# Performance work log

Hardware: AMD Instinct MI355X
Metric: run time of the kernel (lower is better)

The kernel has to match this reference:

```python
import jax, jax.numpy as jnp
import numpy as np

D_MODEL = 256
N_LAYER = 4
D_INNER = 512   # expand=2
D_STATE = 16
DT_RANK = 16    # ceil(d_model/16)
D_CONV = 4
VOCAB = 16
BATCH = 1
SEQLEN = 4096
EPS = 1e-5


def setup_inputs() -> dict:
    key = jax.random.key(0)
    ks = jax.random.split(key, 10)
    s = 0.02
    A_init = jnp.log(jnp.arange(1, D_STATE + 1, dtype=jnp.float32))  # S4D-real init
    return {
        "input_ids": jax.random.randint(ks[0], (BATCH, SEQLEN), 0, VOCAB, dtype=jnp.int32),
        "embed_w": jax.random.normal(ks[1], (VOCAB, D_MODEL), jnp.float32) * s,
        "norm_w": jnp.ones((N_LAYER, D_MODEL), jnp.float32),
        "in_proj_w": jax.random.normal(ks[2], (N_LAYER, 2 * D_INNER, D_MODEL), jnp.float32) * s,
        "out_proj_w": jax.random.normal(ks[3], (N_LAYER, D_MODEL, D_INNER), jnp.float32) * s,
        "conv_w": jax.random.normal(ks[4], (N_LAYER, 2, D_INNER, D_CONV), jnp.float32) * s,
        "conv_b": jnp.zeros((N_LAYER, 2, D_INNER), jnp.float32),
        "x_proj_w": jax.random.normal(ks[5], (N_LAYER, 2, DT_RANK + 2 * D_STATE, D_INNER), jnp.float32) * s,
        "dt_proj_w": jax.random.normal(ks[6], (N_LAYER, 2, D_INNER, DT_RANK), jnp.float32) * s,
        "dt_proj_b": jax.random.normal(ks[7], (N_LAYER, 2, D_INNER), jnp.float32) * 0.1,
        "A_log": jnp.broadcast_to(A_init, (N_LAYER, 2, D_INNER, D_STATE)) + 0.0,
        "Dp": jnp.ones((N_LAYER, 2, D_INNER), jnp.float32),
        "norm_f_w": jnp.ones((D_MODEL,), jnp.float32),
    }


def rmsnorm(x, w):
    return x * jax.lax.rsqrt(jnp.mean(x * x, axis=-1, keepdims=True) + EPS) * w


def selective_scan(u, dt, A, Bm, Cm, Dv):
    # u, dt: (B,L,Di); A: (Di,N); Bm, Cm: (B,L,N); Dv: (Di,)
    dA = jnp.exp(dt[..., None] * A)                         # (B,L,Di,N)
    dBu = dt[..., None] * Bm[:, :, None, :] * u[..., None]  # (B,L,Di,N)

    def step(h, xs):
        dA_t, dBu_t, C_t = xs
        h = dA_t * h + dBu_t                                # (B,Di,N)
        y = jnp.einsum('bdn,bn->bd', h, C_t)
        return h, y

    h0 = jnp.zeros((u.shape[0], D_INNER, D_STATE), u.dtype)
    xs = (jnp.moveaxis(dA, 1, 0), jnp.moveaxis(dBu, 1, 0), jnp.moveaxis(Cm, 1, 0))
    _, ys = jax.lax.scan(step, h0, xs)                      # (L,B,Di)
    return jnp.moveaxis(ys, 0, 1) + u * Dv


def mamba_dir(x, in_w, out_w, cw, cb, xpw, dtw, dtb, a_log, dv):
    # x: (B,L,D)
    xz = jnp.einsum('bld,ed->ble', x, in_w)                 # (B,L,2*Di)
    u, z = jnp.split(xz, 2, axis=-1)
    # causal depthwise conv1d
    uc = jnp.moveaxis(u, 1, 2)                              # (B,Di,L)
    uc = jax.lax.conv_general_dilated(
        uc, cw[:, None, :], (1,), [(D_CONV - 1, 0)],
        feature_group_count=D_INNER, dimension_numbers=('NCH', 'OIH', 'NCH'))
    u = jax.nn.silu(jnp.moveaxis(uc, 1, 2) + cb)            # (B,L,Di)
    xdb = jnp.einsum('bld,ed->ble', u, xpw)                 # (B,L,dt_rank+2N)
    dt_r, Bm, Cm = jnp.split(xdb, [DT_RANK, DT_RANK + D_STATE], axis=-1)
    dt = jax.nn.softplus(jnp.einsum('blr,dr->bld', dt_r, dtw) + dtb)
    A = -jnp.exp(a_log)                                     # (Di,N)
    y = selective_scan(u, dt, A, Bm, Cm, dv)
    y = y * jax.nn.silu(z)
    return jnp.einsum('bld,od->blo', y, out_w)


def reference(input_ids, embed_w, norm_w, in_proj_w, out_proj_w, conv_w, conv_b,
              x_proj_w, dt_proj_w, dt_proj_b, A_log, Dp, norm_f_w):
    h = embed_w[input_ids]                                  # (B,L,D)
    residual = None
    for i in range(N_LAYER):
        residual = h if residual is None else h + residual  # residual_in_fp32
        hn = rmsnorm(residual, norm_w[i])
        out_f = mamba_dir(hn, in_proj_w[i], out_proj_w[i], conv_w[i, 0], conv_b[i, 0],
                          x_proj_w[i, 0], dt_proj_w[i, 0], dt_proj_b[i, 0], A_log[i, 0], Dp[i, 0])
        out_r = mamba_dir(hn[:, ::-1], in_proj_w[i], out_proj_w[i], conv_w[i, 1], conv_b[i, 1],
                          x_proj_w[i, 1], dt_proj_w[i, 1], dt_proj_b[i, 1], A_log[i, 1], Dp[i, 1])[:, ::-1]
        h = out_f + out_r                                   # bidirectional 'add'
    residual = h + residual
    return rmsnorm(residual, norm_f_w)
```

## Files before the change

kernel.cpp:

```cpp
#include <hip/hip_runtime.h>
#include <hip/hip_bf16.h>
#include <math.h>

#define L_  4096
#define D_  256
#define DI_ 512
#define NS_ 16
#define NC_ 128
#define CH_ 32

typedef __attribute__((ext_vector_type(8))) short short8;
typedef __attribute__((ext_vector_type(4))) short short4v;
typedef __attribute__((ext_vector_type(4))) float f32x4;

__global__ __launch_bounds__(256) void prep_kernel(const int* __restrict__ ids,
    const float* __restrict__ ew, const float* __restrict__ inw,
    const float* __restrict__ outw, const float* __restrict__ xpw,
    float* __restrict__ res, __hip_bfloat16* __restrict__ inw_b,
    __hip_bfloat16* __restrict__ outw_b, __hip_bfloat16* __restrict__ xpw_b) {
  int idx = blockIdx.x * 256 + threadIdx.x;
  int l = idx >> 8, d = idx & 255;
  res[idx] = ew[ids[l] * D_ + d];
  inw_b[idx] = __float2bfloat16(inw[idx]);
  {
    int layer = idx >> 18;
    int rem = idx & 262143;
    int o = rem >> 10, k = rem & 1023;
    outw_b[idx] = __float2bfloat16(outw[((size_t)layer * 256 + o) * 512 + (k & 511)]);
  }
  if (idx < 4 * 2 * 64 * 512) {
    int layer = idx >> 16;
    int rem = idx & 65535;
    int dir = rem >> 15;
    int r = (rem >> 9) & 63, k = idx & 511;
    float v = (r < 48) ? xpw[(((size_t)layer * 2 + dir) * 48 + r) * 512 + k] : 0.f;
    xpw_b[idx] = __float2bfloat16(v);
  }
}

template<bool BF16OUT>
__global__ __launch_bounds__(256) void rmsnorm_kernel(float* __restrict__ residual,
    const float* __restrict__ hadd, const float* __restrict__ w, void* __restrict__ out) {
  int row = blockIdx.x * 4 + (threadIdx.x >> 6);
  int lane = threadIdx.x & 63;
  size_t o = (size_t)row * D_ + lane * 4;
  float4 v = *(const float4*)(residual + o);
  if (hadd) {
    float4 a = *(const float4*)(hadd + o);
    v.x += a.x; v.y += a.y; v.z += a.z; v.w += a.w;
    *(float4*)(residual + o) = v;
  }
  float sq = fmaf(v.x, v.x, fmaf(v.y, v.y, fmaf(v.z, v.z, v.w * v.w)));
  #pragma unroll
  for (int s = 32; s > 0; s >>= 1) sq += __shfl_xor(sq, s, 64);
  float scale = rsqrtf(sq * (1.f / D_) + 1e-5f);
  float4 wv = *(const float4*)(w + lane * 4);
  float r0 = v.x * scale * wv.x, r1 = v.y * scale * wv.y;
  float r2 = v.z * scale * wv.z, r3 = v.w * scale * wv.w;
  if (BF16OUT) {
    __hip_bfloat16* ob = (__hip_bfloat16*)out + o;
    short4v s4;
    s4[0] = __bfloat16_as_short(__float2bfloat16(r0));
    s4[1] = __bfloat16_as_short(__float2bfloat16(r1));
    s4[2] = __bfloat16_as_short(__float2bfloat16(r2));
    s4[3] = __bfloat16_as_short(__float2bfloat16(r3));
    *reinterpret_cast<short4v*>(ob) = s4;
  } else {
    float4 r = {r0, r1, r2, r3};
    *((float4*)out + (o >> 2)) = r;
  }
}

__device__ __forceinline__ void gload_lds16(const void* g, void* l) {
  __builtin_amdgcn_global_load_lds((const __attribute__((address_space(1))) unsigned int*)g,
                                   (__attribute__((address_space(3))) unsigned int*)l,
                                   16, 0, 0);
}

template<int BM, int BN, bool BF16OUT>
__global__ __launch_bounds__(256) void gemm_bt_bf16(const __hip_bfloat16* __restrict__ A,
    const __hip_bfloat16* __restrict__ B, void* __restrict__ Cv, int M, int N, int K,
    size_t sA, size_t sB, size_t sC) {
  A += (size_t)blockIdx.z * sA; B += (size_t)blockIdx.z * sB;
  constexpr int FM = (BM / 2) / 16, FN = (BN / 2) / 16;
  constexpr int ABYTES = BM * 64, BBYTES = BN * 64;
  __shared__ __attribute__((aligned(16))) char As[ABYTES];
  __shared__ __attribute__((aligned(16))) char Bs[BBYTES];
  int tid = threadIdx.x, lane = tid & 63, w = tid >> 6;
  int bm = blockIdx.y * BM, bn = blockIdx.x * BN;
  int wr = (w >> 1) * (BM / 2), wc = (w & 1) * (BN / 2);
  f32x4 acc[FM][FN] = {};
  for (int k0 = 0; k0 < K; k0 += 32) {
    __syncthreads();
    #pragma unroll
    for (int i = 0; i < ABYTES / 4096; ++i) {
      int x = (i * 256 + tid) * 16;
      int xs = x ^ (((x >> 7) & 3) << 4);
      int row = xs >> 6, col = (xs & 63) >> 1;
      gload_lds16(A + (size_t)(bm + row) * K + k0 + col, As + i * 4096 + w * 1024);
    }
    #pragma unroll
    for (int i = 0; i < BBYTES / 4096; ++i) {
      int x = (i * 256 + tid) * 16;
      int xs = x ^ (((x >> 7) & 3) << 4);
      int row = xs >> 6, col = (xs & 63) >> 1;
      gload_lds16(B + (size_t)(bn + row) * K + k0 + col, Bs + i * 4096 + w * 1024);
    }
    __syncthreads();
    short8 af[FM], bf[FN];
    #pragma unroll
    for (int m = 0; m < FM; ++m) {
      int row = wr + m * 16 + (lane & 15);
      int x = row * 64 + ((lane >> 4) * 16);
      x ^= ((x >> 7) & 3) << 4;
      af[m] = *reinterpret_cast<const short8*>(As + x);
    }
    #pragma unroll
    for (int n = 0; n < FN; ++n) {
      int row = wc + n * 16 + (lane & 15);
      int x = row * 64 + ((lane >> 4) * 16);
      x ^= ((x >> 7) & 3) << 4;
      bf[n] = *reinterpret_cast<const short8*>(Bs + x);
    }
    #pragma unroll
    for (int m = 0; m < FM; ++m)
      #pragma unroll
      for (int n = 0; n < FN; ++n)
        acc[m][n] = __builtin_amdgcn_mfma_f32_16x16x32_bf16(af[m], bf[n], acc[m][n], 0, 0, 0);
  }
  #pragma unroll
  for (int m = 0; m < FM; ++m)
    #pragma unroll
    for (int n = 0; n < FN; ++n)
      #pragma unroll
      for (int j = 0; j < 4; ++j) {
        size_t off = (size_t)blockIdx.z * sC +
                     (size_t)(bm + wr + m * 16 + (lane >> 4) * 4 + j) * N + bn + wc + n * 16 + (lane & 15);
        if (BF16OUT) ((__hip_bfloat16*)Cv)[off] = __float2bfloat16(acc[m][n][j]);
        else         ((float*)Cv)[off] = acc[m][n][j];
      }
}

__global__ __launch_bounds__(256) void xproj_conv(const __hip_bfloat16* __restrict__ xz,
    const float* __restrict__ cw, const float* __restrict__ cb,
    const __hip_bfloat16* __restrict__ xpw_b, float* __restrict__ xdb) {
  int dir = blockIdx.y;
  int l0 = blockIdx.x * 32;
  int tid = threadIdx.x, lane = tid & 63, w = tid >> 6;
  __shared__ __attribute__((aligned(16))) unsigned short sxz[36][512];
  __shared__ __attribute__((aligned(16))) unsigned short su[32][520];
  __shared__ __attribute__((aligned(16))) char Bs[4096];
  #pragma unroll
  for (int it = 0; it < 9; ++it) {
    int s = it * 4 + w;
    int sc = s > 34 ? 34 : s;
    int f = l0 - 3 + sc;
    int row = dir ? (L_ - 1 - f) : f;
    row = row < 0 ? 0 : (row > L_ - 1 ? L_ - 1 : row);
    gload_lds16((const char*)xz + (size_t)row * 2048 + lane * 16, (char*)sxz + s * 1024);
  }
  __syncthreads();
  #pragma unroll
  for (int half = 0; half < 2; ++half) {
    int ch = half * 256 + tid;
    float4 wv = *(const float4*)(cw + ((size_t)dir * DI_ + ch) * 4);
    float bias = cb[(size_t)dir * DI_ + ch];
    #pragma unroll 4
    for (int t = 0; t < 32; ++t) {
      float acc = bias;
      #pragma unroll
      for (int k = 0; k < 4; ++k) {
        float xv = (l0 == 0 && t + k < 3) ? 0.f
                 : __uint_as_float((unsigned)sxz[t + k][ch] << 16);
        acc = fmaf(((const float*)&wv)[k], xv, acc);
      }
      float uvf = acc * __builtin_amdgcn_rcpf(1.f + __expf(-acc));
      su[t][ch] = (unsigned short)__bfloat16_as_short(__float2bfloat16(uvf));
    }
  }
  const __hip_bfloat16* B = xpw_b + (size_t)dir * 64 * 512;
  int wr = (w >> 1) * 16, wc = (w & 1) * 32;
  f32x4 acc2[2] = {};
  for (int k0 = 0; k0 < 512; k0 += 32) {
    __syncthreads();
    {
      int x = tid * 16;
      int xs = x ^ (((x >> 7) & 3) << 4);
      int row = xs >> 6, col = (xs & 63) >> 1;
      gload_lds16(B + (size_t)row * 512 + k0 + col, Bs + w * 1024);
    }
    __syncthreads();
    short8 af = *reinterpret_cast<const short8*>(
        (const char*)su + (wr + (lane & 15)) * 1040 + (k0 + (lane >> 4) * 8) * 2);
    #pragma unroll
    for (int n = 0; n < 2; ++n) {
      int row = wc + n * 16 + (lane & 15);
      int x = row * 64 + ((lane >> 4) * 16);
      x ^= ((x >> 7) & 3) << 4;
      short8 bf8 = *reinterpret_cast<const short8*>(Bs + x);
      acc2[n] = __builtin_amdgcn_mfma_f32_16x16x32_bf16(af, bf8, acc2[n], 0, 0, 0);
    }
  }
  #pragma unroll
  for (int n = 0; n < 2; ++n)
    #pragma unroll
    for (int j = 0; j < 4; ++j)
      xdb[((size_t)dir * L_ + l0 + wr + (lane >> 4) * 4 + j) * 64 + wc + n * 16 + (lane & 15)]
          = acc2[n][j];
}

__device__ __forceinline__ void scan_stage(int tid, int lane, int w, int q, int dir, int c,
    const float* __restrict__ xdb, const __hip_bfloat16* __restrict__ xz,
    const float* __restrict__ cw, const float* __restrict__ cb,
    const float* __restrict__ dtw, const float* __restrict__ dtbp,
    float (*sxdb)[64], unsigned short (*su)[128], float (*sdt)[128],
    unsigned short (*sxz)[128]) {
  const char* bg = (const char*)(xdb + ((size_t)dir * L_ + (size_t)c * CH_) * 64);
  #pragma unroll
  for (int i = 0; i < 2; ++i)
    gload_lds16(bg + w * 2048 + i * 1024 + lane * 16, (char*)sxdb + w * 2048 + i * 1024);
  #pragma unroll
  for (int it = 0; it < 3; ++it) {
    int b = it * 4 + w;
    if (b < 9) {
      int s = b * 4 + (lane >> 4);
      s = s > 34 ? 34 : s;
      int f = c * CH_ - 3 + s;
      int row = dir ? (L_ - 1 - f) : f;
      row = row < 0 ? 0 : (row > L_ - 1 ? L_ - 1 : row);
      gload_lds16((const char*)xz + (size_t)row * 2048 + q * 256 + (lane & 15) * 16,
                  (char*)sxz + b * 1024);
    }
  }
  __syncthreads();
  {
    int c128 = tid & 127, tp = tid >> 7;
    int ch = q * 128 + c128;
    float4 wv = *(const float4*)(cw + ((size_t)dir * DI_ + ch) * 4);
    float bias = cb[(size_t)dir * DI_ + ch];
    #pragma unroll
    for (int i = 0; i < 16; ++i) {
      int t = tp * 16 + i;
      float acc = bias;
      #pragma unroll
      for (int k = 0; k < 4; ++k) {
        float xv = (c == 0 && t + k < 3) ? 0.f
                 : __uint_as_float((unsigned)sxz[t + k][c128] << 16);
        acc = fmaf(((const float*)&wv)[k], xv, acc);
      }
      float uvf = acc * __builtin_amdgcn_rcpf(1.f + __expf(-acc));
      su[t][c128] = (unsigned short)__bfloat16_as_short(__float2bfloat16(uvf));
    }
  }
  __syncthreads();
  {
    int dlx = tid & 127, tst = tid >> 7;
    int dc = q * 128 + dlx;
    const float4* wr = (const float4*)(dtw + ((size_t)dir * DI_ + dc) * 16);
    float4 w0 = wr[0], w1 = wr[1], w2 = wr[2], w3 = wr[3];
    float bias = dtbp[(size_t)dir * DI_ + dc];
    #pragma unroll
    for (int i = 0; i < 16; ++i) {
      int t = tst + i * 2;
      const float4* xr = (const float4*)&sxdb[t][0];
      float4 x0 = xr[0], x1 = xr[1], x2 = xr[2], x3 = xr[3];
      float acc = bias;
      acc = fmaf(w0.x, x0.x, fmaf(w0.y, x0.y, fmaf(w0.z, x0.z, fmaf(w0.w, x0.w, acc))));
      acc = fmaf(w1.x, x1.x, fmaf(w1.y, x1.y, fmaf(w1.z, x1.z, fmaf(w1.w, x1.w, acc))));
      acc = fmaf(w2.x, x2.x, fmaf(w2.y, x2.y, fmaf(w2.z, x2.z, fmaf(w2.w, x2.w, acc))));
      acc = fmaf(w3.x, x3.x, fmaf(w3.y, x3.y, fmaf(w3.z, x3.z, fmaf(w3.w, x3.w, acc))));
      float e = __expf(fminf(acc, 20.f));
      sdt[t][dlx] = acc > 20.f ? acc : __logf(1.f + e);
    }
  }
  __syncthreads();
}

__global__ __launch_bounds__(256) void scan_pass1(const __hip_bfloat16* __restrict__ xz,
    const float* __restrict__ cw, const float* __restrict__ cb,
    const float* __restrict__ xdb, const float* __restrict__ dtw,
    const float* __restrict__ dtbp, const float* __restrict__ A_log,
    float* __restrict__ Pb, float* __restrict__ Qb) {
  int dir = blockIdx.y;
  int c = blockIdx.x >> 2, q = blockIdx.x & 3;
  int tid = threadIdx.x, lane = tid & 63, w = tid >> 6;
  int dl = tid >> 1, nh = tid & 1;
  int d = q * 128 + dl;
  __shared__ __attribute__((aligned(16))) char smem[32768];
  float (*sxdb)[64] = (float(*)[64])smem;
  unsigned short (*su)[128] = (unsigned short(*)[128])(smem + 8192);
  float (*sdt)[128] = (float(*)[128])(smem + 16384);
  unsigned short (*sxz)[128] = (unsigned short(*)[128])(smem + 16384);
  float Av[8], P[8], Q[8];
  const float4* Ab4 = (const float4*)(A_log + ((size_t)dir * DI_ + d) * 16 + nh * 8);
  float4 a0 = Ab4[0], a1 = Ab4[1];
  float al[8] = {a0.x, a0.y, a0.z, a0.w, a1.x, a1.y, a1.z, a1.w};
  #pragma unroll
  for (int j = 0; j < 8; ++j) { Av[j] = -__expf(al[j]); P[j] = 1.f; Q[j] = 0.f; }
  scan_stage(tid, lane, w, q, dir, c, xdb, xz, cw, cb, dtw, dtbp, sxdb, su, sdt, sxz);
  #pragma unroll 2
  for (int t = 0; t < CH_; ++t) {
    float dtv = sdt[t][dl];
    float uv  = __uint_as_float((unsigned)su[t][dl] << 16);
    float du = dtv * uv;
    const float4* Br = (const float4*)&sxdb[t][16 + nh * 8];
    float4 b0 = Br[0], b1 = Br[1];
    float bb[8] = {b0.x, b0.y, b0.z, b0.w, b1.x, b1.y, b1.z, b1.w};
    #pragma unroll
    for (int j = 0; j < 8; ++j) {
      float dA = __expf(dtv * Av[j]);
      P[j] *= dA;
      Q[j] = fmaf(dA, Q[j], bb[j] * du);
    }
  }
  size_t ob = ((size_t)dir * NC_ + c) * 8192 + (size_t)(nh * 8) * 512 + d;
  #pragma unroll
  for (int j = 0; j < 8; ++j) { Pb[ob + j * 512] = P[j]; Qb[ob + j * 512] = Q[j]; }
}

__global__ __launch_bounds__(64) void scan_combine(const float* __restrict__ Pb,
    const float* __restrict__ Qb, float* __restrict__ H0) {
  int idx = blockIdx.x * 64 + threadIdx.x;
  int dir = idx >> 13; int s = idx & 8191;
  size_t base = (size_t)dir * NC_ * 8192 + s;
  float h = 0.f;
  #pragma unroll 8
  for (int c = 0; c < NC_; ++c) {
    size_t o = base + (size_t)c * 8192;
    H0[o] = h;
    h = fmaf(Pb[o], h, Qb[o]);
  }
}

__global__ __launch_bounds__(256) void scan_pass2(const __hip_bfloat16* __restrict__ xz,
    const float* __restrict__ cw, const float* __restrict__ cb,
    const float* __restrict__ xdb, const float* __restrict__ dtw,
    const float* __restrict__ dtbp, const float* __restrict__ A_log,
    const float* __restrict__ Dp, const float* __restrict__ H0,
    __hip_bfloat16* __restrict__ yg) {
  int dir = blockIdx.y;
  int c = blockIdx.x >> 2, q = blockIdx.x & 3;
  int tid = threadIdx.x, lane = tid & 63, w = tid >> 6;
  int dl = tid >> 1, nh = tid & 1;
  int d = q * 128 + dl;
  __shared__ __attribute__((aligned(16))) char smem[32768];
  float (*sxdb)[64] = (float(*)[64])smem;
  unsigned short (*su)[128] = (unsigned short(*)[128])(smem + 8192);
  float (*sdt)[128] = (float(*)[128])(smem + 16384);
  unsigned short (*sxz)[128] = (unsigned short(*)[128])(smem + 16384);
  float Av[8], h[8];
  const float4* Ab4 = (const float4*)(A_log + ((size_t)dir * DI_ + d) * 16 + nh * 8);
  float4 a0 = Ab4[0], a1 = Ab4[1];
  float al[8] = {a0.x, a0.y, a0.z, a0.w, a1.x, a1.y, a1.z, a1.w};
  size_t ob = ((size_t)dir * NC_ + c) * 8192 + (size_t)(nh * 8) * 512 + d;
  #pragma unroll
  for (int j = 0; j < 8; ++j) { Av[j] = -__expf(al[j]); h[j] = H0[ob + j * 512]; }
  float Dv = Dp[(size_t)dir * DI_ + d];
  scan_stage(tid, lane, w, q, dir, c, xdb, xz, cw, cb, dtw, dtbp, sxdb, su, sdt, sxz);
  #pragma unroll 2
  for (int t = 0; t < CH_; ++t) {
    float dtv = sdt[t][dl];
    float uv  = __uint_as_float((unsigned)su[t][dl] << 16);
    float du = dtv * uv;
    const float4* Br = (const float4*)&sxdb[t][16 + nh * 8];
    const float4* Cr = (const float4*)&sxdb[t][32 + nh * 8];
    float4 b0 = Br[0], b1 = Br[1], c0 = Cr[0], c1 = Cr[1];
    float bb[8] = {b0.x, b0.y, b0.z, b0.w, b1.x, b1.y, b1.z, b1.w};
    float cc[8] = {c0.x, c0.y, c0.z, c0.w, c1.x, c1.y, c1.z, c1.w};
    float y = 0.f;
    #pragma unroll
    for (int j = 0; j < 8; ++j) {
      float dA = __expf(dtv * Av[j]);
      h[j] = fmaf(dA, h[j], bb[j] * du);
      y = fmaf(h[j], cc[j], y);
    }
    y += __shfl_xor(y, 1, 64);
    if (nh == 0) {
      int l = c * CH_ + t;
      int pos = dir ? (L_ - 1 - l) : l;
      float zv = __bfloat162float(xz[(size_t)pos * 1024 + DI_ + d]);
      float g = zv * __builtin_amdgcn_rcpf(1.f + __expf(-zv));
      yg[(size_t)pos * 1024 + (size_t)dir * DI_ + d] = __float2bfloat16((y + uv * Dv) * g);
    }
  }
}

extern "C" void kernel_launch(void* const* d_in, const int* in_sizes, int n_in,
                              void* d_out, int out_size, void* d_ws, size_t ws_size,
                              hipStream_t stream) {
  const int*   ids       = (const int*)  d_in[0];
  const float* embed_w   = (const float*)d_in[1];
  const float* norm_w    = (const float*)d_in[2];
  const float* in_proj_w = (const float*)d_in[3];
  const float* out_proj_w= (const float*)d_in[4];
  const float* conv_w    = (const float*)d_in[5];
  const float* conv_b    = (const float*)d_in[6];
  const float* x_proj_w  = (const float*)d_in[7];
  const float* dt_proj_w = (const float*)d_in[8];
  const float* dt_proj_b = (const float*)d_in[9];
  const float* A_log     = (const float*)d_in[10];
  const float* Dp        = (const float*)d_in[11];
  const float* norm_f_w  = (const float*)d_in[12];

  float* ws = (float*)d_ws;
  float* residual = ws; ws += (size_t)L_ * D_;
  float* xdb      = ws; ws += (size_t)2 * L_ * 64;
  float* hbuf     = ws; ws += (size_t)L_ * D_;
  float* Pb       = ws; ws += (size_t)2 * NC_ * 8192;
  float* Qb       = ws; ws += (size_t)2 * NC_ * 8192;
  float* H0       = ws; ws += (size_t)2 * NC_ * 8192;
  __hip_bfloat16* hn_b   = (__hip_bfloat16*)ws;
  __hip_bfloat16* xz_b   = hn_b + (size_t)L_ * D_;
  __hip_bfloat16* yg_b   = xz_b + (size_t)L_ * 1024;
  __hip_bfloat16* inw_b  = yg_b + (size_t)L_ * 1024;
  __hip_bfloat16* outw_b = inw_b + (size_t)4 * 1024 * D_;
  __hip_bfloat16* xpw_b  = outw_b + (size_t)4 * D_ * 1024;

  prep_kernel<<<L_ * D_ / 256, 256, 0, stream>>>(ids, embed_w, in_proj_w, out_proj_w,
                                                 x_proj_w, residual, inw_b, outw_b, xpw_b);

  for (int i = 0; i < 4; ++i) {
    rmsnorm_kernel<true><<<L_ / 4, 256, 0, stream>>>(residual, i ? hbuf : nullptr,
                                                     norm_w + (size_t)i * D_, hn_b);
    gemm_bt_bf16<128, 64, true><<<dim3(1024 / 64, L_ / 128, 1), 256, 0, stream>>>(
        hn_b, inw_b + (size_t)i * 1024 * D_, xz_b, L_, 1024, D_, 0, 0, 0);
    xproj_conv<<<dim3(L_ / 32, 2), 256, 0, stream>>>(
        xz_b, conv_w + (size_t)i * 2 * DI_ * 4, conv_b + (size_t)i * 2 * DI_,
        xpw_b + (size_t)i * 2 * 64 * DI_, xdb);
    dim3 gsc(NC_ * 4, 2);
    scan_pass1<<<gsc, 256, 0, stream>>>(
        xz_b, conv_w + (size_t)i * 2 * DI_ * 4, conv_b + (size_t)i * 2 * DI_,
        xdb, dt_proj_w + (size_t)i * 2 * DI_ * 16, dt_proj_b + (size_t)i * 2 * DI_,
        A_log + (size_t)i * 2 * DI_ * NS_, Pb, Qb);
    scan_combine<<<256, 64, 0, stream>>>(Pb, Qb, H0);
    scan_pass2<<<gsc, 256, 0, stream>>>(
        xz_b, conv_w + (size_t)i * 2 * DI_ * 4, conv_b + (size_t)i * 2 * DI_,
        xdb, dt_proj_w + (size_t)i * 2 * DI_ * 16, dt_proj_b + (size_t)i * 2 * DI_,
        A_log + (size_t)i * 2 * DI_ * NS_, Dp + (size_t)i * 2 * DI_, H0, yg_b);
    gemm_bt_bf16<64, 64, false><<<dim3(D_ / 64, L_ / 64, 1), 256, 0, stream>>>(
        yg_b, outw_b + (size_t)i * D_ * 1024, hbuf, L_, D_, 1024, 0, 0, 0);
  }

  rmsnorm_kernel<false><<<L_ / 4, 256, 0, stream>>>(residual, hbuf, norm_f_w, d_out);
}
```

Baseline: 440.8 us.

## Materialize conv output and dt in xproj kernel instead of recomputing in scan passes

```diff
diff --git a/kernel.cpp b/kernel.cpp
--- a/kernel.cpp
+++ b/kernel.cpp
@@ -143,13 +143,16 @@
 
 __global__ __launch_bounds__(256) void xproj_conv(const __hip_bfloat16* __restrict__ xz,
     const float* __restrict__ cw, const float* __restrict__ cb,
-    const __hip_bfloat16* __restrict__ xpw_b, float* __restrict__ xdb) {
+    const __hip_bfloat16* __restrict__ xpw_b, const float* __restrict__ dtw,
+    const float* __restrict__ dtbp, float* __restrict__ xdb,
+    __hip_bfloat16* __restrict__ ucb, float* __restrict__ dtg) {
   int dir = blockIdx.y;
   int l0 = blockIdx.x * 32;
   int tid = threadIdx.x, lane = tid & 63, w = tid >> 6;
   __shared__ __attribute__((aligned(16))) unsigned short sxz[36][512];
   __shared__ __attribute__((aligned(16))) unsigned short su[32][520];
   __shared__ __attribute__((aligned(16))) char Bs[4096];
+  __shared__ __attribute__((aligned(16))) float sdtr[32][16];
   #pragma unroll
   for (int it = 0; it < 9; ++it) {
     int s = it * 4 + w;
@@ -160,6 +163,7 @@
     gload_lds16((const char*)xz + (size_t)row * 2048 + lane * 16, (char*)sxz + s * 1024);
   }
   __syncthreads();
+  unsigned short* ucs = (unsigned short*)ucb;
   #pragma unroll
   for (int half = 0; half < 2; ++half) {
     int ch = half * 256 + tid;
@@ -175,7 +179,9 @@
         acc = fmaf(((const float*)&wv)[k], xv, acc);
       }
       float uvf = acc * __builtin_amdgcn_rcpf(1.f + __expf(-acc));
-      su[t][ch] = (unsigned short)__bfloat16_as_short(__float2bfloat16(uvf));
+      unsigned short bits = (unsigned short)__bfloat16_as_short(__float2bfloat16(uvf));
+      su[t][ch] = bits;
+      ucs[((size_t)dir * L_ + l0 + t) * DI_ + ch] = bits;
     }
   }
   const __hip_bfloat16* B = xpw_b + (size_t)dir * 64 * 512;
@@ -207,62 +213,21 @@
     for (int j = 0; j < 4; ++j)
       xdb[((size_t)dir * L_ + l0 + wr + (lane >> 4) * 4 + j) * 64 + wc + n * 16 + (lane & 15)]
           = acc2[n][j];
-}
-
-__device__ __forceinline__ void scan_stage(int tid, int lane, int w, int q, int dir, int c,
-    const float* __restrict__ xdb, const __hip_bfloat16* __restrict__ xz,
-    const float* __restrict__ cw, const float* __restrict__ cb,
-    const float* __restrict__ dtw, const float* __restrict__ dtbp,
-    float (*sxdb)[64], unsigned short (*su)[128], float (*sdt)[128],
-    unsigned short (*sxz)[128]) {
-  const char* bg = (const char*)(xdb + ((size_t)dir * L_ + (size_t)c * CH_) * 64);
-  #pragma unroll
-  for (int i = 0; i < 2; ++i)
-    gload_lds16(bg + w * 2048 + i * 1024 + lane * 16, (char*)sxdb + w * 2048 + i * 1024);
-  #pragma unroll
-  for (int it = 0; it < 3; ++it) {
-    int b = it * 4 + w;
-    if (b < 9) {
-      int s = b * 4 + (lane >> 4);
-      s = s > 34 ? 34 : s;
-      int f = c * CH_ - 3 + s;
-      int row = dir ? (L_ - 1 - f) : f;
-      row = row < 0 ? 0 : (row > L_ - 1 ? L_ - 1 : row);
-      gload_lds16((const char*)xz + (size_t)row * 2048 + q * 256 + (lane & 15) * 16,
-                  (char*)sxz + b * 1024);
-    }
+  if ((w & 1) == 0) {
+    #pragma unroll
+    for (int j = 0; j < 4; ++j)
+      sdtr[wr + (lane >> 4) * 4 + j][lane & 15] = acc2[0][j];
   }
   __syncthreads();
-  {
-    int c128 = tid & 127, tp = tid >> 7;
-    int ch = q * 128 + c128;
-    float4 wv = *(const float4*)(cw + ((size_t)dir * DI_ + ch) * 4);
-    float bias = cb[(size_t)dir * DI_ + ch];
-    #pragma unroll
-    for (int i = 0; i < 16; ++i) {
-      int t = tp * 16 + i;
-      float acc = bias;
-      #pragma unroll
-      for (int k = 0; k < 4; ++k) {
-        float xv = (c == 0 && t + k < 3) ? 0.f
-                 : __uint_as_float((unsigned)sxz[t + k][c128] << 16);
-        acc = fmaf(((const float*)&wv)[k], xv, acc);
-      }
-      float uvf = acc * __builtin_amdgcn_rcpf(1.f + __expf(-acc));
-      su[t][c128] = (unsigned short)__bfloat16_as_short(__float2bfloat16(uvf));
-    }
-  }
-  __syncthreads();
-  {
-    int dlx = tid & 127, tst = tid >> 7;
-    int dc = q * 128 + dlx;
-    const float4* wr = (const float4*)(dtw + ((size_t)dir * DI_ + dc) * 16);
-    float4 w0 = wr[0], w1 = wr[1], w2 = wr[2], w3 = wr[3];
-    float bias = dtbp[(size_t)dir * DI_ + dc];
-    #pragma unroll
-    for (int i = 0; i < 16; ++i) {
-      int t = tst + i * 2;
-      const float4* xr = (const float4*)&sxdb[t][0];
+  #pragma unroll
+  for (int half = 0; half < 2; ++half) {
+    int ch = half * 256 + tid;
+    const float4* wr4 = (const float4*)(dtw + ((size_t)dir * DI_ + ch) * 16);
+    float4 w0 = wr4[0], w1 = wr4[1], w2 = wr4[2], w3 = wr4[3];
+    float bias = dtbp[(size_t)dir * DI_ + ch];
+    #pragma unroll 4
+    for (int t = 0; t < 32; ++t) {
+      const float4* xr = (const float4*)&sdtr[t][0];
       float4 x0 = xr[0], x1 = xr[1], x2 = xr[2], x3 = xr[3];
       float acc = bias;
       acc = fmaf(w0.x, x0.x, fmaf(w0.y, x0.y, fmaf(w0.z, x0.z, fmaf(w0.w, x0.w, acc))));
@@ -270,40 +235,59 @@
       acc = fmaf(w2.x, x2.x, fmaf(w2.y, x2.y, fmaf(w2.z, x2.z, fmaf(w2.w, x2.w, acc))));
       acc = fmaf(w3.x, x3.x, fmaf(w3.y, x3.y, fmaf(w3.z, x3.z, fmaf(w3.w, x3.w, acc))));
       float e = __expf(fminf(acc, 20.f));
-      sdt[t][dlx] = acc > 20.f ? acc : __logf(1.f + e);
-    }
+      dtg[((size_t)dir * L_ + l0 + t) * DI_ + ch] = acc > 20.f ? acc : __logf(1.f + e);
+    }
+  }
+}
+
+__device__ __forceinline__ void scan_stage2(int lane, int w, int q, int dir, int c,
+    const float* __restrict__ xdb, const __hip_bfloat16* __restrict__ uc,
+    const float* __restrict__ dtg,
+    float (*sxbc)[32], unsigned short (*su)[128], float (*sdt)[128]) {
+  const char* bg = (const char*)(xdb + ((size_t)dir * L_ + (size_t)c * CH_) * 64);
+  const char* ug = (const char*)(uc + ((size_t)dir * L_ + (size_t)c * CH_) * DI_ + q * 128);
+  const char* dg = (const char*)(dtg + ((size_t)dir * L_ + (size_t)c * CH_) * DI_ + q * 128);
+  {
+    int unit = w * 64 + lane;
+    gload_lds16(bg + (unit >> 3) * 256 + 64 + (unit & 7) * 16, (char*)sxbc + w * 1024);
+  }
+  #pragma unroll
+  for (int i = 0; i < 2; ++i) {
+    int byte = (w * 128 + i * 64 + lane) * 16;
+    gload_lds16(ug + (byte >> 8) * 1024 + (byte & 255), (char*)su + w * 2048 + i * 1024);
+  }
+  #pragma unroll
+  for (int i = 0; i < 4; ++i) {
+    int byte = (w * 4 + i) * 1024 + lane * 16;
+    gload_lds16(dg + (byte >> 9) * 2048 + (byte & 511), (char*)sdt + (w * 4 + i) * 1024);
   }
   __syncthreads();
 }
 
-__global__ __launch_bounds__(256) void scan_pass1(const __hip_bfloat16* __restrict__ xz,
-    const float* __restrict__ cw, const float* __restrict__ cb,
-    const float* __restrict__ xdb, const float* __restrict__ dtw,
-    const float* __restrict__ dtbp, const float* __restrict__ A_log,
-    float* __restrict__ Pb, float* __restrict__ Qb) {
+__global__ __launch_bounds__(256) void scan_pass1(const __hip_bfloat16* __restrict__ uc,
+    const float* __restrict__ dtg, const float* __restrict__ xdb,
+    const float* __restrict__ A_log, float* __restrict__ Pb, float* __restrict__ Qb) {
   int dir = blockIdx.y;
   int c = blockIdx.x >> 2, q = blockIdx.x & 3;
   int tid = threadIdx.x, lane = tid & 63, w = tid >> 6;
   int dl = tid >> 1, nh = tid & 1;
   int d = q * 128 + dl;
-  __shared__ __attribute__((aligned(16))) char smem[32768];
-  float (*sxdb)[64] = (float(*)[64])smem;
-  unsigned short (*su)[128] = (unsigned short(*)[128])(smem + 8192);
-  float (*sdt)[128] = (float(*)[128])(smem + 16384);
-  unsigned short (*sxz)[128] = (unsigned short(*)[128])(smem + 16384);
+  __shared__ __attribute__((aligned(16))) float sxbc[CH_][32];
+  __shared__ __attribute__((aligned(16))) unsigned short su[CH_][128];
+  __shared__ __attribute__((aligned(16))) float sdt[CH_][128];
   float Av[8], P[8], Q[8];
   const float4* Ab4 = (const float4*)(A_log + ((size_t)dir * DI_ + d) * 16 + nh * 8);
   float4 a0 = Ab4[0], a1 = Ab4[1];
   float al[8] = {a0.x, a0.y, a0.z, a0.w, a1.x, a1.y, a1.z, a1.w};
   #pragma unroll
   for (int j = 0; j < 8; ++j) { Av[j] = -__expf(al[j]); P[j] = 1.f; Q[j] = 0.f; }
-  scan_stage(tid, lane, w, q, dir, c, xdb, xz, cw, cb, dtw, dtbp, sxdb, su, sdt, sxz);
+  scan_stage2(lane, w, q, dir, c, xdb, uc, dtg, sxbc, su, sdt);
   #pragma unroll 2
   for (int t = 0; t < CH_; ++t) {
     float dtv = sdt[t][dl];
     float uv  = __uint_as_float((unsigned)su[t][dl] << 16);
     float du = dtv * uv;
-    const float4* Br = (const float4*)&sxdb[t][16 + nh * 8];
+    const float4* Br = (const float4*)&sxbc[t][nh * 8];
     float4 b0 = Br[0], b1 = Br[1];
     float bb[8] = {b0.x, b0.y, b0.z, b0.w, b1.x, b1.y, b1.z, b1.w};
     #pragma unroll
@@ -332,22 +316,19 @@
   }
 }
 
-__global__ __launch_bounds__(256) void scan_pass2(const __hip_bfloat16* __restrict__ xz,
-    const float* __restrict__ cw, const float* __restrict__ cb,
-    const float* __restrict__ xdb, const float* __restrict__ dtw,
-    const float* __restrict__ dtbp, const float* __restrict__ A_log,
-    const float* __restrict__ Dp, const float* __restrict__ H0,
+__global__ __launch_bounds__(256) void scan_pass2(const __hip_bfloat16* __restrict__ uc,
+    const float* __restrict__ dtg, const float* __restrict__ xdb,
+    const float* __restrict__ A_log, const float* __restrict__ Dp,
+    const __hip_bfloat16* __restrict__ xz, const float* __restrict__ H0,
     __hip_bfloat16* __restrict__ yg) {
   int dir = blockIdx.y;
   int c = blockIdx.x >> 2, q = blockIdx.x & 3;
   int tid = threadIdx.x, lane = tid & 63, w = tid >> 6;
   int dl = tid >> 1, nh = tid & 1;
   int d = q * 128 + dl;
-  __shared__ __attribute__((aligned(16))) char smem[32768];
-  float (*sxdb)[64] = (float(*)[64])smem;
-  unsigned short (*su)[128] = (unsigned short(*)[128])(smem + 8192);
-  float (*sdt)[128] = (float(*)[128])(smem + 16384);
-  unsigned short (*sxz)[128] = (unsigned short(*)[128])(smem + 16384);
+  __shared__ __attribute__((aligned(16))) float sxbc[CH_][32];
+  __shared__ __attribute__((aligned(16))) unsigned short su[CH_][128];
+  __shared__ __attribute__((aligned(16))) float sdt[CH_][128];
   float Av[8], h[8];
   const float4* Ab4 = (const float4*)(A_log + ((size_t)dir * DI_ + d) * 16 + nh * 8);
   float4 a0 = Ab4[0], a1 = Ab4[1];
@@ -356,14 +337,14 @@
   #pragma unroll
   for (int j = 0; j < 8; ++j) { Av[j] = -__expf(al[j]); h[j] = H0[ob + j * 512]; }
   float Dv = Dp[(size_t)dir * DI_ + d];
-  scan_stage(tid, lane, w, q, dir, c, xdb, xz, cw, cb, dtw, dtbp, sxdb, su, sdt, sxz);
+  scan_stage2(lane, w, q, dir, c, xdb, uc, dtg, sxbc, su, sdt);
   #pragma unroll 2
   for (int t = 0; t < CH_; ++t) {
     float dtv = sdt[t][dl];
     float uv  = __uint_as_float((unsigned)su[t][dl] << 16);
     float du = dtv * uv;
-    const float4* Br = (const float4*)&sxdb[t][16 + nh * 8];
-    const float4* Cr = (const float4*)&sxdb[t][32 + nh * 8];
+    const float4* Br = (const float4*)&sxbc[t][nh * 8];
+    const float4* Cr = (const float4*)&sxbc[t][16 + nh * 8];
     float4 b0 = Br[0], b1 = Br[1], c0 = Cr[0], c1 = Cr[1];
     float bb[8] = {b0.x, b0.y, b0.z, b0.w, b1.x, b1.y, b1.z, b1.w};
     float cc[8] = {c0.x, c0.y, c0.z, c0.w, c1.x, c1.y, c1.z, c1.w};
@@ -406,13 +387,15 @@
   float* residual = ws; ws += (size_t)L_ * D_;
   float* xdb      = ws; ws += (size_t)2 * L_ * 64;
   float* hbuf     = ws; ws += (size_t)L_ * D_;
+  float* dtg      = ws; ws += (size_t)2 * L_ * DI_;
   float* Pb       = ws; ws += (size_t)2 * NC_ * 8192;
   float* Qb       = ws; ws += (size_t)2 * NC_ * 8192;
   float* H0       = ws; ws += (size_t)2 * NC_ * 8192;
   __hip_bfloat16* hn_b   = (__hip_bfloat16*)ws;
   __hip_bfloat16* xz_b   = hn_b + (size_t)L_ * D_;
   __hip_bfloat16* yg_b   = xz_b + (size_t)L_ * 1024;
-  __hip_bfloat16* inw_b  = yg_b + (size_t)L_ * 1024;
+  __hip_bfloat16* uc_b   = yg_b + (size_t)L_ * 1024;
+  __hip_bfloat16* inw_b  = uc_b + (size_t)2 * L_ * DI_;
   __hip_bfloat16* outw_b = inw_b + (size_t)4 * 1024 * D_;
   __hip_bfloat16* xpw_b  = outw_b + (size_t)4 * D_ * 1024;
 
@@ -426,17 +409,15 @@
         hn_b, inw_b + (size_t)i * 1024 * D_, xz_b, L_, 1024, D_, 0, 0, 0);
     xproj_conv<<<dim3(L_ / 32, 2), 256, 0, stream>>>(
         xz_b, conv_w + (size_t)i * 2 * DI_ * 4, conv_b + (size_t)i * 2 * DI_,
-        xpw_b + (size_t)i * 2 * 64 * DI_, xdb);
+        xpw_b + (size_t)i * 2 * 64 * DI_, dt_proj_w + (size_t)i * 2 * DI_ * 16,
+        dt_proj_b + (size_t)i * 2 * DI_, xdb, uc_b, dtg);
     dim3 gsc(NC_ * 4, 2);
     scan_pass1<<<gsc, 256, 0, stream>>>(
-        xz_b, conv_w + (size_t)i * 2 * DI_ * 4, conv_b + (size_t)i * 2 * DI_,
-        xdb, dt_proj_w + (size_t)i * 2 * DI_ * 16, dt_proj_b + (size_t)i * 2 * DI_,
-        A_log + (size_t)i * 2 * DI_ * NS_, Pb, Qb);
+        uc_b, dtg, xdb, A_log + (size_t)i * 2 * DI_ * NS_, Pb, Qb);
     scan_combine<<<256, 64, 0, stream>>>(Pb, Qb, H0);
     scan_pass2<<<gsc, 256, 0, stream>>>(
-        xz_b, conv_w + (size_t)i * 2 * DI_ * 4, conv_b + (size_t)i * 2 * DI_,
-        xdb, dt_proj_w + (size_t)i * 2 * DI_ * 16, dt_proj_b + (size_t)i * 2 * DI_,
-        A_log + (size_t)i * 2 * DI_ * NS_, Dp + (size_t)i * 2 * DI_, H0, yg_b);
+        uc_b, dtg, xdb, A_log + (size_t)i * 2 * DI_ * NS_, Dp + (size_t)i * 2 * DI_,
+        xz_b, H0, yg_b);
     gemm_bt_bf16<64, 64, false><<<dim3(D_ / 64, L_ / 64, 1), 256, 0, stream>>>(
         yg_b, outw_b + (size_t)i * D_ * 1024, hbuf, L_, D_, 1024, 0, 0, 0);
   }
```

Measured after the change: 452.0 us. 2.5% more time.
